# Optimization experiments

Hardware: AMD Instinct MI355X
Metric: run time of the kernel (lower is better)

## Reference

```python
import jax, jax.numpy as jnp
import numpy as np
import math

NUM_POINTS = 64
OUTPUT_DIMS = 128
MINVAL = -1.0
MAXVAL = 1.0
WINDOW_SIZE = 8.0


def setup_inputs() -> dict:
    key = jax.random.key(0)
    k1, k2 = jax.random.split(key)
    # continuous feature values in [minval, maxval]
    x = jax.random.uniform(k1, (64, 8192), dtype=jnp.float32, minval=MINVAL, maxval=MAXVAL)
    embeddings = jax.random.normal(k2, (NUM_POINTS, OUTPUT_DIMS), dtype=jnp.float32)
    return {"x": x, "embeddings": embeddings}


def _rect_window(d, window_size):
    w_2 = window_size / 2
    return (jnp.sign(d + w_2) - jnp.sign(d - w_2)) * 0.5


def _hann_window(d, window_size):
    y = jnp.cos(jnp.float32(math.pi) * d / window_size)
    return y * y * _rect_window(d, window_size)


def reference(x, embeddings):
    # map x from [minval, maxval] to grid coordinates [0, num_points]
    scale = jnp.float32(NUM_POINTS / (MAXVAL - MINVAL))
    xs = (x - jnp.float32(MINVAL)) * scale
    points = jnp.arange(NUM_POINTS, dtype=jnp.float32)
    # [B, S, num_points] distance to each grid point
    d = xs[..., None] - points
    w = _hann_window(d, jnp.float32(WINDOW_SIZE))
    # normalized: divide_no_nan semantics (0 where row-sum == 0)
    s = jnp.sum(w, axis=-1, keepdims=True)
    w = jnp.where(s == 0, jnp.float32(0), w / jnp.where(s == 0, jnp.float32(1), s))
    # [B, S, output_dims]
    return jnp.einsum('bsp,pd->bsd', w, embeddings)
```

## Files before the change

### kernel.cpp

```cpp
#include <hip/hip_runtime.h>
#include <math.h>

#define NUM_POINTS 64
#define OUT_DIMS 128
#define BLOCK_THREADS 256
#define ELEMS_PER_BLOCK 256

__global__ __launch_bounds__(BLOCK_THREADS) void ce_kernel(
    const float* __restrict__ x,
    const float* __restrict__ emb,
    float* __restrict__ out) {
  __shared__ float s_emb[NUM_POINTS * OUT_DIMS];
  {
    float4* s4 = (float4*)s_emb;
    const float4* e4 = (const float4*)emb;
    const int t = threadIdx.x;
#pragma unroll
    for (int i = 0; i < (NUM_POINTS * OUT_DIMS / 4) / BLOCK_THREADS; ++i)
      s4[t + i * BLOCK_THREADS] = e4[t + i * BLOCK_THREADS];
  }
  __syncthreads();

  const int tid = threadIdx.x;
  const int lane_chunk = tid & 31;
  const int sub = tid >> 5;
  const int base = blockIdx.x * ELEMS_PER_BLOCK;

#pragma unroll 1
  for (int it = 0; it < ELEMS_PER_BLOCK / 8; ++it) {
    const int e = base + it * 8 + sub;
    const float xv = x[e];
    const float xs = (xv + 1.0f) * 32.0f;
    const int p0 = (int)floorf(xs) - 3;

    float w[8];
    float wsum = 0.0f;
#pragma unroll
    for (int j = 0; j < 8; ++j) {
      const int p = p0 + j;
      const float d = xs - (float)p;
      const float c = __builtin_amdgcn_cosf(d * 0.0625f);
      float wv = c * c;
      wv = (p >= 0 && p < NUM_POINTS) ? wv : 0.0f;
      w[j] = wv;
      wsum += wv;
    }
    const float inv = (wsum != 0.0f) ? __builtin_amdgcn_rcpf(wsum) : 0.0f;
#pragma unroll
    for (int j = 0; j < 8; ++j) w[j] *= inv;

    float4 acc = make_float4(0.f, 0.f, 0.f, 0.f);
#pragma unroll
    for (int j = 0; j < 8; ++j) {
      int p = p0 + j;
      p = (p < 0) ? 0 : ((p > NUM_POINTS - 1) ? NUM_POINTS - 1 : p);
      const float4 ev = ((const float4*)(s_emb + p * OUT_DIMS))[lane_chunk];
      acc.x = fmaf(w[j], ev.x, acc.x);
      acc.y = fmaf(w[j], ev.y, acc.y);
      acc.z = fmaf(w[j], ev.z, acc.z);
      acc.w = fmaf(w[j], ev.w, acc.w);
    }
    ((float4*)(out + (size_t)e * OUT_DIMS))[lane_chunk] = acc;
  }
}

extern "C" void kernel_launch(void* const* d_in, const int* in_sizes, int n_in,
                              void* d_out, int out_size, void* d_ws, size_t ws_size,
                              hipStream_t stream) {
  const float* x = (const float*)d_in[0];
  const float* emb = (const float*)d_in[1];
  float* out = (float*)d_out;

  const int n = in_sizes[0];
  const int blocks = n / ELEMS_PER_BLOCK;
  ce_kernel<<<blocks, BLOCK_THREADS, 0, stream>>>(x, emb, out);
}
```

Baseline: 300.8 us.

## Compute Hann weights in closed form with padded LDS table and wider per-thread output

Replaces eight per-point cosine evaluations and the per-element normalisation with a single sin/cos pair. Interior weights are derived analytically from the identity that shifted squared cosines sum to a constant, and renormalisation is done only near the grid edges. The embedding table in LDS gets zero pad rows so index clamping disappears. x is staged through LDS, and each thread now produces two float4 outputs per element with a partially unrolled loop. This cuts transcendental and ALU work, at the cost of relying on the analytic weight identity for accuracy.

```diff
diff --git a/kernel.cpp b/kernel.cpp
--- a/kernel.cpp
+++ b/kernel.cpp
@@ -5,62 +5,88 @@
 #define OUT_DIMS 128
 #define BLOCK_THREADS 256
 #define ELEMS_PER_BLOCK 256
+#define PAD_LO 4
+#define PAD_HI 4
+#define LDS_ROWS (NUM_POINTS + PAD_LO + PAD_HI)
 
 __global__ __launch_bounds__(BLOCK_THREADS) void ce_kernel(
     const float* __restrict__ x,
     const float* __restrict__ emb,
     float* __restrict__ out) {
-  __shared__ float s_emb[NUM_POINTS * OUT_DIMS];
+  __shared__ float s_emb[LDS_ROWS * OUT_DIMS];
+  __shared__ float s_x[ELEMS_PER_BLOCK];
+
+  const int tid = threadIdx.x;
   {
-    float4* s4 = (float4*)s_emb;
+    float4* s4 = (float4*)(s_emb + PAD_LO * OUT_DIMS);
     const float4* e4 = (const float4*)emb;
-    const int t = threadIdx.x;
 #pragma unroll
     for (int i = 0; i < (NUM_POINTS * OUT_DIMS / 4) / BLOCK_THREADS; ++i)
-      s4[t + i * BLOCK_THREADS] = e4[t + i * BLOCK_THREADS];
+      s4[tid + i * BLOCK_THREADS] = e4[tid + i * BLOCK_THREADS];
+    if (tid < (PAD_LO * OUT_DIMS / 4)) {
+      ((float4*)s_emb)[tid] = make_float4(0.f, 0.f, 0.f, 0.f);
+      ((float4*)(s_emb + (PAD_LO + NUM_POINTS) * OUT_DIMS))[tid] =
+          make_float4(0.f, 0.f, 0.f, 0.f);
+    }
+    s_x[tid] = x[blockIdx.x * ELEMS_PER_BLOCK + tid];
   }
   __syncthreads();
 
-  const int tid = threadIdx.x;
-  const int lane_chunk = tid & 31;
-  const int sub = tid >> 5;
-  const int base = blockIdx.x * ELEMS_PER_BLOCK;
+  const int chunk = tid & 15;
+  const int sub = tid >> 4;
+  const size_t base = (size_t)blockIdx.x * ELEMS_PER_BLOCK;
+  const float RS2 = 0.70710678118654752f;
 
-#pragma unroll 1
-  for (int it = 0; it < ELEMS_PER_BLOCK / 8; ++it) {
-    const int e = base + it * 8 + sub;
-    const float xv = x[e];
+#pragma unroll 2
+  for (int it = 0; it < ELEMS_PER_BLOCK / 16; ++it) {
+    const int e_local = it * 16 + sub;
+    const float xv = s_x[e_local];
     const float xs = (xv + 1.0f) * 32.0f;
     const int p0 = (int)floorf(xs) - 3;
+    const float t = xs - (float)p0;
+    const float rev = t * 0.125f;
+    const float c4 = 0.125f * __builtin_amdgcn_cosf(rev);
+    const float s4 = 0.125f * __builtin_amdgcn_sinf(rev);
+    const float u4 = RS2 * (c4 + s4);
+    const float v4 = RS2 * (c4 - s4);
 
     float w[8];
-    float wsum = 0.0f;
+    w[0] = 0.125f + c4;  w[1] = 0.125f + u4;
+    w[2] = 0.125f + s4;  w[3] = 0.125f - v4;
+    w[4] = 0.125f - c4;  w[5] = 0.125f - u4;
+    w[6] = 0.125f - s4;  w[7] = 0.125f + v4;
+
+    if (__builtin_expect((unsigned)p0 > 56u, 0)) {
+      float ssum = 0.f;
+#pragma unroll
+      for (int j = 0; j < 8; ++j) {
+        w[j] = ((unsigned)(p0 + j) < 64u) ? w[j] : 0.f;
+        ssum += w[j];
+      }
+      const float inv = __builtin_amdgcn_rcpf(ssum);
+#pragma unroll
+      for (int j = 0; j < 8; ++j) w[j] *= inv;
+    }
+
+    const float* rowbase = s_emb + (p0 + PAD_LO) * OUT_DIMS + chunk * 4;
+    float4 a0 = make_float4(0.f, 0.f, 0.f, 0.f);
+    float4 a1 = make_float4(0.f, 0.f, 0.f, 0.f);
 #pragma unroll
     for (int j = 0; j < 8; ++j) {
-      const int p = p0 + j;
-      const float d = xs - (float)p;
-      const float c = __builtin_amdgcn_cosf(d * 0.0625f);
-      float wv = c * c;
-      wv = (p >= 0 && p < NUM_POINTS) ? wv : 0.0f;
-      w[j] = wv;
-      wsum += wv;
+      const float4 e0 = *(const float4*)(rowbase + j * OUT_DIMS);
+      const float4 e1 = *(const float4*)(rowbase + j * OUT_DIMS + 64);
+      a0.x = fmaf(w[j], e0.x, a0.x);
+      a0.y = fmaf(w[j], e0.y, a0.y);
+      a0.z = fmaf(w[j], e0.z, a0.z);
+      a0.w = fmaf(w[j], e0.w, a0.w);
+      a1.x = fmaf(w[j], e1.x, a1.x);
+      a1.y = fmaf(w[j], e1.y, a1.y);
+      a1.z = fmaf(w[j], e1.z, a1.z);
+      a1.w = fmaf(w[j], e1.w, a1.w);
     }
-    const float inv = (wsum != 0.0f) ? __builtin_amdgcn_rcpf(wsum) : 0.0f;
-#pragma unroll
-    for (int j = 0; j < 8; ++j) w[j] *= inv;
-
-    float4 acc = make_float4(0.f, 0.f, 0.f, 0.f);
-#pragma unroll
-    for (int j = 0; j < 8; ++j) {
-      int p = p0 + j;
-      p = (p < 0) ? 0 : ((p > NUM_POINTS - 1) ? NUM_POINTS - 1 : p);
-      const float4 ev = ((const float4*)(s_emb + p * OUT_DIMS))[lane_chunk];
-      acc.x = fmaf(w[j], ev.x, acc.x);
-      acc.y = fmaf(w[j], ev.y, acc.y);
-      acc.z = fmaf(w[j], ev.z, acc.z);
-      acc.w = fmaf(w[j], ev.w, acc.w);
-    }
-    ((float4*)(out + (size_t)e * OUT_DIMS))[lane_chunk] = acc;
+    float* op = out + (base + e_local) * (size_t)OUT_DIMS + chunk * 4;
+    *(float4*)op = a0;
+    *(float4*)(op + 64) = a1;
   }
 }
 
```

Measured after the change: 268.8 us. -10.6%, faster.
